# Optimization experiments

Measured on AMD Instinct MI355X. Metric: run time of the kernel, lower is better.

## Reference

```python
import jax, jax.numpy as jnp
import numpy as np

N_EMBD = 384
N_HEAD = 6
HEAD_SIZE = N_EMBD // N_HEAD  # 64
B, T = 128, 256
EPS = 1e-5


def setup_inputs() -> dict:
    key = jax.random.key(0)
    ks = jax.random.split(key, 12)
    s = 0.02
    return {
        "x": jax.random.normal(ks[0], (B, T, N_EMBD), dtype=jnp.float32),
        "Wk": jax.random.normal(ks[1], (N_EMBD, N_EMBD), dtype=jnp.float32) * s,
        "Wq": jax.random.normal(ks[2], (N_EMBD, N_EMBD), dtype=jnp.float32) * s,
        "Wv": jax.random.normal(ks[3], (N_EMBD, N_EMBD), dtype=jnp.float32) * s,
        "Wo": jax.random.normal(ks[4], (N_EMBD, N_EMBD), dtype=jnp.float32) * s,
        "bo": jnp.zeros((N_EMBD,), dtype=jnp.float32),
        "W1": jax.random.normal(ks[5], (N_EMBD, 4 * N_EMBD), dtype=jnp.float32) * s,
        "b1": jnp.zeros((4 * N_EMBD,), dtype=jnp.float32),
        "W2": jax.random.normal(ks[6], (4 * N_EMBD, N_EMBD), dtype=jnp.float32) * s,
        "b2": jnp.zeros((N_EMBD,), dtype=jnp.float32),
        "g1": jnp.ones((N_EMBD,), dtype=jnp.float32),
        "be1": jnp.zeros((N_EMBD,), dtype=jnp.float32),
        "g2": jnp.ones((N_EMBD,), dtype=jnp.float32),
        "be2": jnp.zeros((N_EMBD,), dtype=jnp.float32),
    }


def _layernorm(x, g, b):
    mu = jnp.mean(x, axis=-1, keepdims=True)
    var = jnp.var(x, axis=-1, keepdims=True)
    return (x - mu) * jax.lax.rsqrt(var + EPS) * g + b


def _attention(x, Wk, Wq, Wv, Wo, bo):
    Bb, Tt, C = x.shape
    H, D = N_HEAD, HEAD_SIZE
    k = (x @ Wk).reshape(Bb, Tt, H, D).transpose(0, 2, 1, 3)  # (B,H,T,D)
    q = (x @ Wq).reshape(Bb, Tt, H, D).transpose(0, 2, 1, 3)
    v = (x @ Wv).reshape(Bb, Tt, H, D).transpose(0, 2, 1, 3)
    wei = jnp.einsum("bhqd,bhkd->bhqk", q, k) * (D ** -0.5)  # (B,H,T,T)
    mask = jnp.tril(jnp.ones((Tt, Tt), dtype=bool))
    wei = jnp.where(mask, wei, -jnp.inf)
    wei = jax.nn.softmax(wei, axis=-1)
    out = jnp.einsum("bhqk,bhkd->bhqd", wei, v)
    out = out.transpose(0, 2, 1, 3).reshape(Bb, Tt, H * D)
    return out @ Wo + bo


def reference(x, Wk, Wq, Wv, Wo, bo, W1, b1, W2, b2, g1, be1, g2, be2):
    # dropout is identity in eval mode
    h = _layernorm(x, g1, be1)
    x = x + _attention(h, Wk, Wq, Wv, Wo, bo)
    h = _layernorm(x, g2, be2)
    ff = jax.nn.relu(h @ W1 + b1) @ W2 + b2
    return x + ff
```

## Files before the change

kernel.cpp:

```cpp
#include <hip/hip_runtime.h>

typedef unsigned short u16;
typedef short s16x8 __attribute__((ext_vector_type(8)));
typedef float f32x4 __attribute__((ext_vector_type(4)));

__device__ inline u16 f2bf(float f) {
    unsigned u = __float_as_uint(f);
    u += 0x7FFF + ((u >> 16) & 1);
    return (u16)(u >> 16);
}
__device__ inline float bf2f(u16 h) {
    return __uint_as_float((unsigned)h << 16);
}

__device__ inline f32x4 mfma16(s16x8 a, s16x8 b, f32x4 c) {
    return __builtin_amdgcn_mfma_f32_16x16x32_bf16(a, b, c, 0, 0, 0);
}

__device__ __forceinline__ void gl16(const u16* g, u16* l) {
    __builtin_amdgcn_global_load_lds(
        (const __attribute__((address_space(1))) void*)g,
        (__attribute__((address_space(3))) void*)l, 16, 0, 0);
}

__global__ __launch_bounds__(256) void tcvt_all(
    const float* __restrict__ Wq, const float* __restrict__ Wk,
    const float* __restrict__ Wv, const float* __restrict__ Wo,
    const float* __restrict__ W1, const float* __restrict__ W2,
    u16* __restrict__ wT) {
    __shared__ float tile[32][33];
    int bid = blockIdx.x;
    const float* src;
    u16* dst;
    int K, N, tk, tn;
    if (bid < 576) {
        int m = bid / 144, t = bid - m * 144;
        src = m == 0 ? Wq : m == 1 ? Wk : m == 2 ? Wv : Wo;
        dst = wT + m * 147456;
        K = 384; N = 384; tk = t / 12; tn = t - (t / 12) * 12;
    } else if (bid < 1152) {
        int t = bid - 576;
        src = W1; dst = wT + 589824;
        K = 384; N = 1536; tk = t / 48; tn = t - (t / 48) * 48;
    } else {
        int t = bid - 1152;
        src = W2; dst = wT + 1179648;
        K = 1536; N = 384; tk = t / 12; tn = t - (t / 12) * 12;
    }
    int tx = threadIdx.x & 31, ty = threadIdx.x >> 5;
#pragma unroll
    for (int p = 0; p < 4; ++p) {
        int k = tk * 32 + ty + p * 8;
        tile[ty + p * 8][tx] = src[(size_t)k * N + tn * 32 + tx];
    }
    __syncthreads();
#pragma unroll
    for (int p = 0; p < 4; ++p) {
        int n = tn * 32 + ty + p * 8;
        dst[(size_t)n * K + tk * 32 + tx] = f2bf(tile[tx][ty + p * 8]);
    }
}

__global__ __launch_bounds__(256) void ln_kernel(const float* __restrict__ x,
                                                 const float* __restrict__ g,
                                                 const float* __restrict__ be,
                                                 u16* __restrict__ out) {
    int lane = threadIdx.x & 63;
    int w = threadIdx.x >> 6;
    int row = blockIdx.x * 4 + w;
    const float* xr = x + (size_t)row * 384;
    float v[6];
    float s = 0.f, sq = 0.f;
#pragma unroll
    for (int i = 0; i < 6; ++i) {
        v[i] = xr[i * 64 + lane];
        s += v[i];
        sq += v[i] * v[i];
    }
#pragma unroll
    for (int m = 1; m < 64; m <<= 1) {
        s += __shfl_xor(s, m);
        sq += __shfl_xor(sq, m);
    }
    float mu = s * (1.0f / 384.0f);
    float var = sq * (1.0f / 384.0f) - mu * mu;
    float rstd = rsqrtf(var + 1e-5f);
    u16* orow = out + (size_t)row * 384;
#pragma unroll
    for (int i = 0; i < 6; ++i) {
        int col = i * 64 + lane;
        orow[col] = f2bf((v[i] - mu) * rstd * g[col] + be[col]);
    }
}

__global__ __launch_bounds__(256) void ln_bf16_kernel(const u16* __restrict__ x,
                                                      const float* __restrict__ g,
                                                      const float* __restrict__ be,
                                                      u16* __restrict__ out) {
    int lane = threadIdx.x & 63;
    int w = threadIdx.x >> 6;
    int row = blockIdx.x * 4 + w;
    const u16* xr = x + (size_t)row * 384;
    bool act = lane < 48;
    float v[8];
    float s = 0.f, sq = 0.f;
    if (act) {
        s16x8 t = *(const s16x8*)&xr[lane * 8];
#pragma unroll
        for (int j = 0; j < 8; ++j) {
            v[j] = bf2f((u16)t[j]);
            s += v[j];
            sq += v[j] * v[j];
        }
    }
#pragma unroll
    for (int m = 1; m < 64; m <<= 1) {
        s += __shfl_xor(s, m);
        sq += __shfl_xor(sq, m);
    }
    float mu = s * (1.0f / 384.0f);
    float var = sq * (1.0f / 384.0f) - mu * mu;
    float rstd = rsqrtf(var + 1e-5f);
    if (act) {
        float4 g0 = *(const float4*)&g[lane * 8];
        float4 g1 = *(const float4*)&g[lane * 8 + 4];
        float4 b0 = *(const float4*)&be[lane * 8];
        float4 b1 = *(const float4*)&be[lane * 8 + 4];
        float gg[8] = {g0.x, g0.y, g0.z, g0.w, g1.x, g1.y, g1.z, g1.w};
        float bb[8] = {b0.x, b0.y, b0.z, b0.w, b1.x, b1.y, b1.z, b1.w};
        u16* orow = out + (size_t)row * 384 + lane * 8;
#pragma unroll
        for (int j = 0; j < 8; ++j)
            orow[j] = f2bf((v[j] - mu) * rstd * gg[j] + bb[j]);
    }
}

template <int BIAS, int RELU, int RES, int RESBF, int OBF16, int NBN>
__global__ __launch_bounds__(512, 4) void gemm_kernel(const u16* __restrict__ A,
                                                      const u16* __restrict__ Bt,
                                                      const float* __restrict__ bias,
                                                      const void* __restrict__ res,
                                                      void* __restrict__ out,
                                                      int M, int N, int K) {
    __shared__ u16 La[2][256 * 32];
    __shared__ u16 Lb[2][128 * 32];
    int tid = threadIdx.x;
    int lane = tid & 63, w = tid >> 6;
    int wm = w >> 1, wn = w & 1;
    int lr = lane & 15, lg = lane >> 4;

    int nwg = gridDim.x;
    int q = nwg >> 3, r = nwg & 7;
    int xcd = blockIdx.x & 7, lin = blockIdx.x >> 3;
    int wg = (xcd < r ? xcd * (q + 1) : r * (q + 1) + (xcd - r) * q) + lin;
    int bx = wg % NBN, by = wg / NBN;
    int m0 = by * 256, n0 = bx * 128;

    int rsub = lane >> 2;
    int gslot = ((lane & 3) ^ ((lane >> 3) & 3)) * 8;
    const u16* pa[2];
    const u16* pb1;
#pragma unroll
    for (int i = 0; i < 2; ++i)
        pa[i] = A + (size_t)(m0 + w * 32 + i * 16 + rsub) * K + gslot;
    pb1 = Bt + (size_t)(n0 + w * 16 + rsub) * K + gslot;

    f32x4 acc[4][4];
    f32x4 zero = {0.f, 0.f, 0.f, 0.f};
#pragma unroll
    for (int mt = 0; mt < 4; ++mt)
#pragma unroll
        for (int nt = 0; nt < 4; ++nt) acc[mt][nt] = zero;

    int sel = (lg ^ ((lr >> 1) & 3)) << 3;
    int nt_steps = K >> 5;

#define STAGE(t, bsel)                                  \
    do {                                                \
        int kc = (t) << 5;                              \
        gl16(pa[0] + kc, &La[bsel][(w * 32) * 32]);     \
        gl16(pa[1] + kc, &La[bsel][(w * 32 + 16) * 32]);\
        gl16(pb1 + kc, &Lb[bsel][(w * 16) * 32]);       \
    } while (0)

    STAGE(0, 0);

    for (int t = 0; t < nt_steps; ++t) {
        asm volatile("s_waitcnt vmcnt(0)" ::: "memory");
        __builtin_amdgcn_s_barrier();
        asm volatile("" ::: "memory");
        if (t + 1 < nt_steps) STAGE(t + 1, (t + 1) & 1);
        const u16* lab = La[t & 1];
        const u16* lbb = Lb[t & 1];
        s16x8 af[4], bfr[4];
#pragma unroll
        for (int mt = 0; mt < 4; ++mt)
            af[mt] = *(const s16x8*)&lab[(wm * 64 + mt * 16 + lr) * 32 + sel];
#pragma unroll
        for (int nt = 0; nt < 4; ++nt)
            bfr[nt] = *(const s16x8*)&lbb[(wn * 64 + nt * 16 + lr) * 32 + sel];
        __builtin_amdgcn_s_setprio(1);
#pragma unroll
        for (int mt = 0; mt < 4; ++mt)
#pragma unroll
            for (int nt = 0; nt < 4; ++nt)
                acc[mt][nt] = mfma16(af[mt], bfr[nt], acc[mt][nt]);
        __builtin_amdgcn_s_setprio(0);
    }
#undef STAGE

#pragma unroll
    for (int mt = 0; mt < 4; ++mt) {
#pragma unroll
        for (int nt = 0; nt < 4; ++nt) {
            int m_base = m0 + wm * 64 + mt * 16 + lg * 4;
            int n = n0 + wn * 64 + nt * 16 + lr;
            float bv = BIAS ? bias[n] : 0.0f;
#pragma unroll
            for (int r2 = 0; r2 < 4; ++r2) {
                size_t idx = (size_t)(m_base + r2) * N + n;
                float val = acc[mt][nt][r2] + bv;
                if (RES) {
                    if (RESBF)
                        val += bf2f(((const u16*)res)[idx]);
                    else
                        val += ((const float*)res)[idx];
                }
                if (RELU) val = fmaxf(val, 0.0f);
                if (OBF16)
                    ((u16*)out)[idx] = f2bf(val);
                else
                    ((float*)out)[idx] = val;
            }
        }
    }
}

template <int QT0>
__global__ __launch_bounds__(512) void attn_kernel(const u16* __restrict__ qkv,
                                                   u16* __restrict__ aout) {
    constexpr int NT = QT0 ? 8 : 16;
    constexpr int TL = NT * 16;
    constexpr int VTW = TL + 8;
    constexpr int NSTG = QT0 ? 2 : 4;
    __shared__ u16 Kl[TL * 72];
    __shared__ u16 Vt[64 * VTW];
    __shared__ u16 Pl[8 * 16 * VTW];
    int h = blockIdx.x, b = blockIdx.y;
    int tid = threadIdx.x, lane = tid & 63, w = tid >> 6;
    int lr = lane & 15, lg = lane >> 4;
    const u16* qb = qkv + (size_t)b * 256 * 1152;

#pragma unroll
    for (int i = 0; i < NSTG; ++i) {
        int c = tid + i * 512;
        int t = c >> 3, dch = c & 7;
        *(int4*)&Kl[t * 72 + dch * 8] =
            *(const int4*)(qb + (size_t)t * 1152 + 384 + h * 64 + dch * 8);
        union { int4 v; u16 u[8]; } vv;
        vv.v = *(const int4*)(qb + (size_t)t * 1152 + 768 + h * 64 + dch * 8);
#pragma unroll
        for (int j = 0; j < 8; ++j) Vt[(dch * 8 + j) * VTW + t] = vv.u[j];
    }

    const int q0 = QT0 ? 0 : 128;
    const u16* qrow = qb + (size_t)(q0 + w * 16 + lr) * 1152 + h * 64;
    s16x8 qf0 = *(const s16x8*)(qrow + lg * 8);
    s16x8 qf1 = *(const s16x8*)(qrow + 32 + lg * 8);

    __syncthreads();

    f32x4 zero = {0.f, 0.f, 0.f, 0.f};
    f32x4 s[NT];
#pragma unroll
    for (int nt = 0; nt < NT; ++nt) s[nt] = zero;
#pragma unroll
    for (int nt = 0; nt < NT; ++nt) {
        s16x8 kf0 = *(const s16x8*)&Kl[(nt * 16 + lr) * 72 + lg * 8];
        s16x8 kf1 = *(const s16x8*)&Kl[(nt * 16 + lr) * 72 + 32 + lg * 8];
        s[nt] = mfma16(qf0, kf0, s[nt]);
        s[nt] = mfma16(qf1, kf1, s[nt]);
    }

    int ib = q0 + w * 16 + lg * 4;
    float mx[4] = {-1e30f, -1e30f, -1e30f, -1e30f};
#pragma unroll
    for (int nt = 0; nt < NT; ++nt) {
        int jg = nt * 16 + lr;
#pragma unroll
        for (int r = 0; r < 4; ++r) {
            float val = s[nt][r] * 0.125f;
            val = (jg <= ib + r) ? val : -1e30f;
            s[nt][r] = val;
            mx[r] = fmaxf(mx[r], val);
        }
    }
#pragma unroll
    for (int r = 0; r < 4; ++r) {
        mx[r] = fmaxf(mx[r], __shfl_xor(mx[r], 1));
        mx[r] = fmaxf(mx[r], __shfl_xor(mx[r], 2));
        mx[r] = fmaxf(mx[r], __shfl_xor(mx[r], 4));
        mx[r] = fmaxf(mx[r], __shfl_xor(mx[r], 8));
    }
    float rs[4] = {0.f, 0.f, 0.f, 0.f};
#pragma unroll
    for (int nt = 0; nt < NT; ++nt) {
#pragma unroll
        for (int r = 0; r < 4; ++r) {
            float p = __expf(s[nt][r] - mx[r]);
            s[nt][r] = p;
            rs[r] += p;
        }
    }
#pragma unroll
    for (int r = 0; r < 4; ++r) {
        rs[r] += __shfl_xor(rs[r], 1);
        rs[r] += __shfl_xor(rs[r], 2);
        rs[r] += __shfl_xor(rs[r], 4);
        rs[r] += __shfl_xor(rs[r], 8);
    }
    u16* Pw = &Pl[w * 16 * VTW];
#pragma unroll
    for (int nt = 0; nt < NT; ++nt)
#pragma unroll
        for (int r = 0; r < 4; ++r)
            Pw[(lg * 4 + r) * VTW + nt * 16 + lr] = f2bf(s[nt][r]);

    f32x4 o[4];
#pragma unroll
    for (int nt = 0; nt < 4; ++nt) o[nt] = zero;
#pragma unroll
    for (int kc = 0; kc < NT / 2; ++kc) {
        s16x8 pf = *(const s16x8*)&Pw[lr * VTW + kc * 32 + lg * 8];
#pragma unroll
        for (int nt = 0; nt < 4; ++nt) {
            s16x8 vf = *(const s16x8*)&Vt[(nt * 16 + lr) * VTW + kc * 32 + lg * 8];
            o[nt] = mfma16(pf, vf, o[nt]);
        }
    }
    float inv[4];
#pragma unroll
    for (int r = 0; r < 4; ++r) inv[r] = 1.0f / rs[r];
    u16* ob = aout + (size_t)(b * 256 + q0 + w * 16) * 384 + h * 64;
#pragma unroll
    for (int nt = 0; nt < 4; ++nt)
#pragma unroll
        for (int r = 0; r < 4; ++r)
            ob[(size_t)(lg * 4 + r) * 384 + nt * 16 + lr] = f2bf(o[nt][r] * inv[r]);
}

extern "C" void kernel_launch(void* const* d_in, const int* in_sizes, int n_in,
                              void* d_out, int out_size, void* d_ws, size_t ws_size,
                              hipStream_t stream) {
    const float* x   = (const float*)d_in[0];
    const float* Wk  = (const float*)d_in[1];
    const float* Wq  = (const float*)d_in[2];
    const float* Wv  = (const float*)d_in[3];
    const float* Wo  = (const float*)d_in[4];
    const float* bo  = (const float*)d_in[5];
    const float* W1  = (const float*)d_in[6];
    const float* b1  = (const float*)d_in[7];
    const float* W2  = (const float*)d_in[8];
    const float* b2  = (const float*)d_in[9];
    const float* g1  = (const float*)d_in[10];
    const float* be1 = (const float*)d_in[11];
    const float* g2  = (const float*)d_in[12];
    const float* be2 = (const float*)d_in[13];

    char* ws = (char*)d_ws;
    u16* hbuf = (u16*)(ws + 0);
    u16* qkv  = (u16*)(ws + 25165824);
    u16* ao   = (u16*)(ws + 100663296);
    u16* x1   = (u16*)(ws + 125829120);
    u16* ubuf = (u16*)(ws + 25165824);
    u16* wT   = (u16*)(ws + 150994944);
    u16* wqkvT = wT;
    u16* woT   = wT + 442368;
    u16* w1T   = woT + 147456;
    u16* w2T   = w1T + 589824;

    tcvt_all<<<1728, 256, 0, stream>>>(Wq, Wk, Wv, Wo, W1, W2, wT);

    ln_kernel<<<8192, 256, 0, stream>>>(x, g1, be1, hbuf);
    gemm_kernel<0, 0, 0, 0, 1, 9><<<1152, 512, 0, stream>>>(
        hbuf, wqkvT, nullptr, nullptr, qkv, 32768, 1152, 384);
    attn_kernel<0><<<dim3(6, 128), 512, 0, stream>>>(qkv, ao);
    attn_kernel<1><<<dim3(6, 128), 512, 0, stream>>>(qkv, ao);
    gemm_kernel<1, 0, 1, 0, 1, 3><<<384, 512, 0, stream>>>(
        ao, woT, bo, x, x1, 32768, 384, 384);
    ln_bf16_kernel<<<8192, 256, 0, stream>>>(x1, g2, be2, hbuf);
    gemm_kernel<1, 1, 0, 0, 1, 12><<<1536, 512, 0, stream>>>(
        hbuf, w1T, b1, nullptr, ubuf, 32768, 1536, 384);
    gemm_kernel<1, 0, 1, 1, 0, 3><<<384, 512, 0, stream>>>(
        ubuf, w2T, b2, x1, (float*)d_out, 32768, 384, 1536);
}
```

Before: 245.2 us.

## Read K fragments from global memory and chunk P staging to cut LDS use

The attention kernel no longer stages K in shared memory. Each wave loads its K MFMA fragments directly from global memory, and the first barrier is moved later so that QK^T starts before V staging completes. The probability matrix is written to a smaller per-wave buffer in 128-column chunks that alternate with the PV MFMAs. Together these roughly halve LDS per block so more blocks can reside per CU, at the cost of redundant global K reads across waves and extra per-chunk LDS traffic.

```diff
diff --git a/kernel.cpp b/kernel.cpp
--- a/kernel.cpp
+++ b/kernel.cpp
@@ -242,10 +242,10 @@
     constexpr int NT = QT0 ? 8 : 16;
     constexpr int TL = NT * 16;
     constexpr int VTW = TL + 8;
+    constexpr int PW = 136;
     constexpr int NSTG = QT0 ? 2 : 4;
-    __shared__ u16 Kl[TL * 72];
     __shared__ u16 Vt[64 * VTW];
-    __shared__ u16 Pl[8 * 16 * VTW];
+    __shared__ u16 Pl[8 * 16 * PW];
     int h = blockIdx.x, b = blockIdx.y;
     int tid = threadIdx.x, lane = tid & 63, w = tid >> 6;
     int lr = lane & 15, lg = lane >> 4;
@@ -255,8 +255,6 @@
     for (int i = 0; i < NSTG; ++i) {
         int c = tid + i * 512;
         int t = c >> 3, dch = c & 7;
-        *(int4*)&Kl[t * 72 + dch * 8] =
-            *(const int4*)(qb + (size_t)t * 1152 + 384 + h * 64 + dch * 8);
         union { int4 v; u16 u[8]; } vv;
         vv.v = *(const int4*)(qb + (size_t)t * 1152 + 768 + h * 64 + dch * 8);
 #pragma unroll
@@ -268,16 +266,15 @@
     s16x8 qf0 = *(const s16x8*)(qrow + lg * 8);
     s16x8 qf1 = *(const s16x8*)(qrow + 32 + lg * 8);
 
-    __syncthreads();
-
     f32x4 zero = {0.f, 0.f, 0.f, 0.f};
     f32x4 s[NT];
 #pragma unroll
     for (int nt = 0; nt < NT; ++nt) s[nt] = zero;
 #pragma unroll
     for (int nt = 0; nt < NT; ++nt) {
-        s16x8 kf0 = *(const s16x8*)&Kl[(nt * 16 + lr) * 72 + lg * 8];
-        s16x8 kf1 = *(const s16x8*)&Kl[(nt * 16 + lr) * 72 + 32 + lg * 8];
+        const u16* krow = qb + (size_t)(nt * 16 + lr) * 1152 + 384 + h * 64;
+        s16x8 kf0 = *(const s16x8*)(krow + lg * 8);
+        s16x8 kf1 = *(const s16x8*)(krow + 32 + lg * 8);
         s[nt] = mfma16(qf0, kf0, s[nt]);
         s[nt] = mfma16(qf1, kf1, s[nt]);
     }
@@ -319,25 +316,35 @@
         rs[r] += __shfl_xor(rs[r], 4);
         rs[r] += __shfl_xor(rs[r], 8);
     }
-    u16* Pw = &Pl[w * 16 * VTW];
-#pragma unroll
-    for (int nt = 0; nt < NT; ++nt)
-#pragma unroll
-        for (int r = 0; r < 4; ++r)
-            Pw[(lg * 4 + r) * VTW + nt * 16 + lr] = f2bf(s[nt][r]);
-
+
+    __syncthreads();
+
+    u16* Pw = &Pl[w * 16 * PW];
     f32x4 o[4];
 #pragma unroll
     for (int nt = 0; nt < 4; ++nt) o[nt] = zero;
 #pragma unroll
-    for (int kc = 0; kc < NT / 2; ++kc) {
-        s16x8 pf = *(const s16x8*)&Pw[lr * VTW + kc * 32 + lg * 8];
-#pragma unroll
-        for (int nt = 0; nt < 4; ++nt) {
-            s16x8 vf = *(const s16x8*)&Vt[(nt * 16 + lr) * VTW + kc * 32 + lg * 8];
-            o[nt] = mfma16(pf, vf, o[nt]);
-        }
-    }
+    for (int p = 0; p < NT / 8; ++p) {
+#pragma unroll
+        for (int j = 0; j < 8; ++j) {
+            int nt = p * 8 + j;
+            int col = j * 16 + lr;
+#pragma unroll
+            for (int r = 0; r < 4; ++r)
+                Pw[(lg * 4 + r) * PW + col] = f2bf(s[nt][r]);
+        }
+#pragma unroll
+        for (int kc = 0; kc < 4; ++kc) {
+            s16x8 pf = *(const s16x8*)&Pw[lr * PW + kc * 32 + lg * 8];
+            int kcv = p * 4 + kc;
+#pragma unroll
+            for (int ntv = 0; ntv < 4; ++ntv) {
+                s16x8 vf = *(const s16x8*)&Vt[(ntv * 16 + lr) * VTW + kcv * 32 + lg * 8];
+                o[ntv] = mfma16(pf, vf, o[ntv]);
+            }
+        }
+    }
+
     float inv[4];
 #pragma unroll
     for (int r = 0; r < 4; ++r) inv[r] = 1.0f / rs[r];
```

New measurement: 253.4 us. 3.4% more time.

## Add 256x192-tile 12-wave GEMM kernel for QKV and FFN1 projections

Applied to the files above, without the earlier changes.

Introduces a new GEMM kernel that uses 768-thread workgroups and 256x192 output tiles. Each of the 12 waves computes a 64x64 sub-tile and also loads part of the A or B tile into double-buffered LDS. It applies an XCD-aware block remapping and replaces the previous QKV and W1 GEMM launches. The larger tile is meant to raise operand reuse per LDS load and cut the number of workgroups, at the cost of more LDS per block and possibly lower occupancy.

```diff
diff --git a/kernel.cpp b/kernel.cpp
--- a/kernel.cpp
+++ b/kernel.cpp
@@ -236,6 +236,114 @@
     }
 }
 
+template <int BIAS, int RELU, int OBF16, int NBN>
+__global__ __launch_bounds__(768, 2) void gemm12_kernel(const u16* __restrict__ A,
+                                                        const u16* __restrict__ Bt,
+                                                        const float* __restrict__ bias,
+                                                        void* __restrict__ out,
+                                                        int M, int N, int K) {
+    __shared__ u16 La[2][256 * 32];
+    __shared__ u16 Lb[2][192 * 32];
+    int tid = threadIdx.x;
+    int lane = tid & 63, w = tid >> 6;
+    int wm = w & 3, wn = w >> 2;
+    int lr = lane & 15, lg = lane >> 4;
+
+    int nwg = gridDim.x;
+    int q = nwg >> 3, r = nwg & 7;
+    int xcd = blockIdx.x & 7, lin = blockIdx.x >> 3;
+    int wg = (xcd < r ? xcd * (q + 1) : r * (q + 1) + (xcd - r) * q) + lin;
+    int bx = wg % NBN, by = wg / NBN;
+    int m0 = by * 256, n0 = bx * 192;
+
+    int rsub = lane >> 2;
+    int gslot = ((lane & 3) ^ ((lane >> 3) & 3)) * 8;
+    const u16* ps[3];
+    int lofs[3];
+    int nld;
+    if (w < 8) {
+        nld = 2;
+#pragma unroll
+        for (int i = 0; i < 2; ++i) {
+            ps[i] = A + (size_t)(m0 + w * 32 + i * 16 + rsub) * K + gslot;
+            lofs[i] = (w * 32 + i * 16) * 32;
+        }
+        ps[2] = A; lofs[2] = 0;
+    } else {
+        nld = 3;
+#pragma unroll
+        for (int i = 0; i < 3; ++i) {
+            ps[i] = Bt + (size_t)(n0 + (w - 8) * 48 + i * 16 + rsub) * K + gslot;
+            lofs[i] = ((w - 8) * 48 + i * 16) * 32;
+        }
+    }
+
+    f32x4 acc[4][4];
+    f32x4 zero = {0.f, 0.f, 0.f, 0.f};
+#pragma unroll
+    for (int mt = 0; mt < 4; ++mt)
+#pragma unroll
+        for (int nt = 0; nt < 4; ++nt) acc[mt][nt] = zero;
+
+    int sel = (lg ^ ((lr >> 1) & 3)) << 3;
+    int nt_steps = K >> 5;
+
+#define STAGE12(t, bsel)                                        \
+    do {                                                        \
+        int kc = (t) << 5;                                      \
+        u16* base = (w < 8) ? La[bsel] : Lb[bsel];              \
+        _Pragma("unroll")                                       \
+        for (int i = 0; i < 3; ++i)                             \
+            if (i < nld) gl16(ps[i] + kc, base + lofs[i]);      \
+    } while (0)
+
+    STAGE12(0, 0);
+
+    for (int t = 0; t < nt_steps; ++t) {
+        asm volatile("s_waitcnt vmcnt(0)" ::: "memory");
+        __builtin_amdgcn_s_barrier();
+        asm volatile("" ::: "memory");
+        if (t + 1 < nt_steps) STAGE12(t + 1, (t + 1) & 1);
+        const u16* lab = La[t & 1];
+        const u16* lbb = Lb[t & 1];
+        s16x8 af[4], bfr[4];
+#pragma unroll
+        for (int mt = 0; mt < 4; ++mt)
+            af[mt] = *(const s16x8*)&lab[(wm * 64 + mt * 16 + lr) * 32 + sel];
+#pragma unroll
+        for (int nt = 0; nt < 4; ++nt)
+            bfr[nt] = *(const s16x8*)&lbb[(wn * 64 + nt * 16 + lr) * 32 + sel];
+        __builtin_amdgcn_s_setprio(1);
+#pragma unroll
+        for (int mt = 0; mt < 4; ++mt)
+#pragma unroll
+            for (int nt = 0; nt < 4; ++nt)
+                acc[mt][nt] = mfma16(af[mt], bfr[nt], acc[mt][nt]);
+        __builtin_amdgcn_s_setprio(0);
+    }
+#undef STAGE12
+
+#pragma unroll
+    for (int mt = 0; mt < 4; ++mt) {
+#pragma unroll
+        for (int nt = 0; nt < 4; ++nt) {
+            int m_base = m0 + wm * 64 + mt * 16 + lg * 4;
+            int n = n0 + wn * 64 + nt * 16 + lr;
+            float bv = BIAS ? bias[n] : 0.0f;
+#pragma unroll
+            for (int r2 = 0; r2 < 4; ++r2) {
+                size_t idx = (size_t)(m_base + r2) * N + n;
+                float val = acc[mt][nt][r2] + bv;
+                if (RELU) val = fmaxf(val, 0.0f);
+                if (OBF16)
+                    ((u16*)out)[idx] = f2bf(val);
+                else
+                    ((float*)out)[idx] = val;
+            }
+        }
+    }
+}
+
 template <int QT0>
 __global__ __launch_bounds__(512) void attn_kernel(const u16* __restrict__ qkv,
                                                    u16* __restrict__ aout) {
@@ -382,15 +490,15 @@
     tcvt_all<<<1728, 256, 0, stream>>>(Wq, Wk, Wv, Wo, W1, W2, wT);
 
     ln_kernel<<<8192, 256, 0, stream>>>(x, g1, be1, hbuf);
-    gemm_kernel<0, 0, 0, 0, 1, 9><<<1152, 512, 0, stream>>>(
-        hbuf, wqkvT, nullptr, nullptr, qkv, 32768, 1152, 384);
+    gemm12_kernel<0, 0, 1, 6><<<768, 768, 0, stream>>>(
+        hbuf, wqkvT, nullptr, qkv, 32768, 1152, 384);
     attn_kernel<0><<<dim3(6, 128), 512, 0, stream>>>(qkv, ao);
     attn_kernel<1><<<dim3(6, 128), 512, 0, stream>>>(qkv, ao);
     gemm_kernel<1, 0, 1, 0, 1, 3><<<384, 512, 0, stream>>>(
         ao, woT, bo, x, x1, 32768, 384, 384);
     ln_bf16_kernel<<<8192, 256, 0, stream>>>(x1, g2, be2, hbuf);
-    gemm_kernel<1, 1, 0, 0, 1, 12><<<1536, 512, 0, stream>>>(
-        hbuf, w1T, b1, nullptr, ubuf, 32768, 1536, 384);
+    gemm12_kernel<1, 1, 1, 8><<<1024, 768, 0, stream>>>(
+        hbuf, w1T, b1, ubuf, 32768, 1536, 384);
     gemm_kernel<1, 0, 1, 1, 0, 3><<<384, 512, 0, stream>>>(
         ubuf, w2T, b2, x1, (float*)d_out, 32768, 384, 1536);
 }
```

Result: no change. 248.8 us (+1.5%).
